# Kernel optimization log

Hardware: AMD Instinct MI355X
Metric: run time of the kernel (lower is better)

Reference implementation:

```python
import jax, jax.numpy as jnp
import numpy as np

N_HEAD = 12
NUM_CLUSTERS = 512
SCALE_FACTOR = 0.5
COEF_PRO = 0.3
EPS_COS = 1e-8


def _ln(x, g, b, eps=1e-5):
    m = jnp.mean(x, -1, keepdims=True)
    v = jnp.mean((x - m) ** 2, -1, keepdims=True)
    return (x - m) / jnp.sqrt(v + eps) * g + b


def _bn_gelu(y, g, b, eps=1e-5):
    # BatchNorm1d (training-mode batch stats) + exact GELU on (N, C)
    m = jnp.mean(y, 0)
    v = jnp.mean((y - m) ** 2, 0)
    return jax.nn.gelu((y - m) / jnp.sqrt(v + eps) * g + b, approximate=False)


def _quick_gelu(x):
    return x * jax.nn.sigmoid(1.702 * x)


def _seg_maxmean(f, idx, n):
    cnt = jax.ops.segment_sum(jnp.ones(f.shape[0], f.dtype), idx, n)
    s = jax.ops.segment_sum(f, idx, n)
    mx = jax.ops.segment_max(f, idx, n)
    mx = jnp.where(cnt[:, None] > 0, mx, 0.0)  # empty segments -> 0 (torch_scatter convention)
    mn = s / jnp.maximum(cnt, 1.0)[:, None]
    return mx, mn


def _cos(a, b):
    na = jnp.maximum(jnp.linalg.norm(a, axis=-1), EPS_COS)
    nb = jnp.maximum(jnp.linalg.norm(b, axis=-1), EPS_COS)
    return jnp.sum(a * b, -1) / (na * nb)


def _block(x, cluster, flat_grid_index, mask, grid_shape,
           ln1_g, ln1_b, w_qkv, b_qkv, w_o, b_o,
           ln2_g, ln2_b, w_fc, b_fc, w_proj, b_proj,
           w_down, b_down, w_up, b_up, bn3d_g, bn3d_b,
           n3_g, n3_b, vw_qkv, vb_qkv, vw_o, vb_o, bn1d_g, bn1d_b):
    B, S, C = x.shape
    G = S - 1
    Dh = C // N_HEAD
    # ---- multi-head self attention ----
    h = _ln(x, ln1_g, ln1_b)
    q, k, v = jnp.split(h @ w_qkv + b_qkv, 3, axis=-1)
    q = q.reshape(B, S, N_HEAD, Dh)
    k = k.reshape(B, S, N_HEAD, Dh)
    v = v.reshape(B, S, N_HEAD, Dh)
    scores = jnp.einsum('bqhd,bkhd->bhqk', q, k) / np.sqrt(Dh).astype(np.float32)
    attn = jax.nn.softmax(scores, -1)
    ao = jnp.einsum('bhqk,bkhd->bqhd', attn, v).reshape(B, S, C) @ w_o + b_o
    attn_weight = attn.mean(axis=1)  # averaged over heads, as need_weights=True
    x = x + ao
    # ---- MLP (QuickGELU) + adapter ----
    h2 = _ln(x, ln2_g, ln2_b)
    ffn = _quick_gelu(h2 @ w_fc + b_fc) @ w_proj + b_proj
    adp = jax.nn.gelu(ffn @ w_down + b_down, approximate=False) @ w_up + b_up
    x = x + ffn + SCALE_FACTOR * adp
    # ---- 3D cluster pooling ----
    cls_x = x[:, 0]
    xt = x[:, 1:]
    feat = xt.reshape(-1, C)
    mx, mn = _seg_maxmean(feat, cluster, NUM_CLUSTERS)
    x3d = _bn_gelu(mx + mn, bn3d_g, bn3d_b)[cluster].reshape(B, G, C)
    # ---- per-view 1D attention + grid scatter pooling ----
    V = mask.shape[0]
    D1 = B * grid_shape
    pos = []
    for i in range(V):
        y = _ln(feat, n3_g[i], n3_b[i]).reshape(B, G, C)
        q1, k1, v1 = jnp.split(y @ vw_qkv[i] + vb_qkv[i], 3, axis=-1)
        s1 = jnp.einsum('bqc,bkc->bqk', q1, k1) / np.sqrt(C).astype(np.float32)
        s1 = jnp.where(mask[i][:, None, :], s1, -1e9)
        a1 = jax.nn.softmax(s1, -1)
        o1 = jnp.einsum('bqk,bkc->bqc', a1, v1) @ vw_o[i] + vb_o[i]
        fx = o1.reshape(-1, C) + feat
        gi = flat_grid_index[i]
        mx1, mn1 = _seg_maxmean(fx, gi, D1)
        d2 = _bn_gelu(mn1 + mx1, bn1d_g[i], bn1d_b[i])[gi].reshape(B, G, C)
        pos.append(d2)
    x_sup = jnp.stack(pos, 0)                                   # (V,B,G,C)
    sims = jnp.stack([(_cos(p, x3d) + 1.0) / 2.0 for p in pos], 0)  # (V,B,G)
    sims = sims / sims.sum(0, keepdims=True)
    x_sup_w = jnp.einsum('vbg,vbgc->bgc', sims, x_sup)
    xt = xt + COEF_PRO * x_sup_w
    out = jnp.concatenate([cls_x[:, None], xt], 1)
    return out, attn_weight


def setup_inputs():
    B, S, C, V = 8, 1025, 768, 6
    GRID = 196
    G = S - 1
    key = jax.random.key(0)
    ks = iter(jax.random.split(key, 64))
    def w(shape):
        return jax.random.normal(next(ks), shape, jnp.float32) * 0.02
    return dict(
        x=jax.random.normal(next(ks), (B, S, C), jnp.float32),
        center1=jax.random.normal(next(ks), (B, V, 3), jnp.float32),
        cluster=jax.random.randint(next(ks), (B * G,), 0, NUM_CLUSTERS),
        flat_grid_index=jax.random.randint(next(ks), (V, B * G), 0, B * GRID),
        mask=jnp.ones((V, B, G), bool),
        grid_shape=GRID,
        ln1_g=jnp.ones(C), ln1_b=jnp.zeros(C),
        w_qkv=w((C, 3 * C)), b_qkv=jnp.zeros(3 * C),
        w_o=w((C, C)), b_o=jnp.zeros(C),
        ln2_g=jnp.ones(C), ln2_b=jnp.zeros(C),
        w_fc=w((C, 4 * C)), b_fc=jnp.zeros(4 * C),
        w_proj=w((4 * C, C)), b_proj=jnp.zeros(C),
        w_down=w((C, 16)), b_down=jnp.zeros(16),
        w_up=w((16, C)), b_up=jnp.zeros(C),
        bn3d_g=jnp.ones(C), bn3d_b=jnp.zeros(C),
        n3_g=jnp.ones((V, C)), n3_b=jnp.zeros((V, C)),
        vw_qkv=w((V, C, 3 * C)), vb_qkv=jnp.zeros((V, 3 * C)),
        vw_o=w((V, C, C)), vb_o=jnp.zeros((V, C)),
        bn1d_g=jnp.ones((V, C)), bn1d_b=jnp.zeros((V, C)),
    )


def reference(x, center1, cluster, flat_grid_index, mask, grid_shape,
              ln1_g, ln1_b, w_qkv, b_qkv, w_o, b_o,
              ln2_g, ln2_b, w_fc, b_fc, w_proj, b_proj,
              w_down, b_down, w_up, b_up, bn3d_g, bn3d_b,
              n3_g, n3_b, vw_qkv, vb_qkv, vw_o, vb_o, bn1d_g, bn1d_b):
    del center1  # only its shape (num_view) is used; V taken from mask
    return _block(x, cluster, flat_grid_index, mask, int(grid_shape),
                  ln1_g, ln1_b, w_qkv, b_qkv, w_o, b_o,
                  ln2_g, ln2_b, w_fc, b_fc, w_proj, b_proj,
                  w_down, b_down, w_up, b_up, bn3d_g, bn3d_b,
                  n3_g, n3_b, vw_qkv, vb_qkv, vw_o, vb_o, bn1d_g, bn1d_b)
```

## Files before the change

kernel.cpp:

```cpp
#include <hip/hip_runtime.h>
#include <math.h>
#include <float.h>

#define BATCH   8
#define SEQ     1025
#define GTOK    1024
#define CDIM    768
#define NHEAD   12
#define DHEAD   64
#define NVIEW   6
#define NCLUST  512
#define NGRID   1568
#define NROWS   8200
#define NFEAT   8192
#define SEGCAP  2048
#define LDT     1032
#define HG      3

typedef unsigned short bf16;
typedef __attribute__((ext_vector_type(8))) short bf16x8;
typedef __attribute__((ext_vector_type(4))) float f32x4;

__device__ __forceinline__ float b2f(bf16 u) {
    union { unsigned int i; float f; } v; v.i = ((unsigned int)u) << 16; return v.f;
}
__device__ __forceinline__ bf16 f2b(float f) {
    union { float f; unsigned int i; } v; v.f = f;
    unsigned int x = v.i;
    return (bf16)((x + 0x7fffu + ((x >> 16) & 1u)) >> 16);
}

__device__ __forceinline__ float block_reduce_sum(float v, float* red) {
    int tid = threadIdx.x;
    red[tid] = v; __syncthreads();
    for (int s = blockDim.x >> 1; s > 0; s >>= 1) {
        if (tid < s) red[tid] += red[tid + s];
        __syncthreads();
    }
    float r = red[0]; __syncthreads();
    return r;
}

__device__ __forceinline__ float brs_fast(float v, float* red4, int nw) {
    #pragma unroll
    for (int o = 32; o > 0; o >>= 1) v += __shfl_down(v, o);
    int lane = threadIdx.x & 63, wid = threadIdx.x >> 6;
    if (lane == 0) red4[wid] = v;
    __syncthreads();
    float r = 0.f;
    for (int i = 0; i < nw; ++i) r += red4[i];
    __syncthreads();
    return r;
}
__device__ __forceinline__ float brm_fast(float v, float* red4, int nw) {
    #pragma unroll
    for (int o = 32; o > 0; o >>= 1) v = fmaxf(v, __shfl_down(v, o));
    int lane = threadIdx.x & 63, wid = threadIdx.x >> 6;
    if (lane == 0) red4[wid] = v;
    __syncthreads();
    float r = -FLT_MAX;
    for (int i = 0; i < nw; ++i) r = fmaxf(r, red4[i]);
    __syncthreads();
    return r;
}

__device__ __forceinline__ float gelu_exact(float v) {
    return 0.5f * v * (1.f + erff(v * 0.70710678118654752f));
}
__device__ __forceinline__ float quick_gelu(float v) {
    return v / (1.f + expf(-1.702f * v));
}

__device__ __forceinline__ long long rmap(long long j, int remap) {
    return remap ? (j + 1 + (j >> 10)) : j;
}

__global__ __launch_bounds__(256)
void transpose_kernel(const float* __restrict__ W, bf16* __restrict__ WT, int K, int N)
{
    __shared__ float t[32][33];
    int n0 = blockIdx.x * 32, k0 = blockIdx.y * 32;
    int tx = threadIdx.x & 31, ty = threadIdx.x >> 5;
    #pragma unroll
    for (int i = 0; i < 4; ++i) {
        int k = k0 + ty + i * 8, n = n0 + tx;
        t[ty + i * 8][tx] = (k < K && n < N) ? W[(long long)k * N + n] : 0.f;
    }
    __syncthreads();
    #pragma unroll
    for (int i = 0; i < 4; ++i) {
        int n = n0 + ty + i * 8, k = k0 + tx;
        if (n < N && k < K)
            WT[(long long)n * K + k] = f2b(t[tx][ty + i * 8]);
    }
}

__global__ __launch_bounds__(256)
void transpose_bf16_kernel(const bf16* __restrict__ src, bf16* __restrict__ dst,
                           int K, int N, int lds, int ldd,
                           long long sSrc, long long sDst)
{
    __shared__ bf16 t[32][34];
    int z = blockIdx.z;
    const bf16* S = src + (long long)z * sSrc;
    bf16* D = dst + (long long)z * sDst;
    int n0 = blockIdx.x * 32, k0 = blockIdx.y * 32;
    int tx = threadIdx.x & 31, ty = threadIdx.x >> 5;
    #pragma unroll
    for (int i = 0; i < 4; ++i) {
        int k = k0 + ty + i * 8, n = n0 + tx;
        t[ty + i * 8][tx] = (k < K && n < N) ? S[(long long)k * lds + n] : (bf16)0;
    }
    __syncthreads();
    #pragma unroll
    for (int i = 0; i < 4; ++i) {
        int n = n0 + ty + i * 8, k = k0 + tx;
        if (n < N && k < K)
            D[(long long)n * ldd + k] = t[tx][ty + i * 8];
    }
}

__global__ __launch_bounds__(256)
void ln_kernel(const float* __restrict__ x, const float* __restrict__ g,
               const float* __restrict__ b, long long goff, bf16* __restrict__ out,
               int remap)
{
    __shared__ float red4[4];
    long long row = blockIdx.x;
    int tid = threadIdx.x;
    long long ibase = rmap(row, remap) * CDIM;
    long long obase = row * CDIM;
    float v0 = x[ibase + tid], v1 = x[ibase + tid + 256], v2 = x[ibase + tid + 512];
    float mean = brs_fast(v0 + v1 + v2, red4, 4) * (1.f / CDIM);
    float d0 = v0 - mean, d1 = v1 - mean, d2 = v2 - mean;
    float var = brs_fast(d0 * d0 + d1 * d1 + d2 * d2, red4, 4) * (1.f / CDIM);
    float rstd = rsqrtf(var + 1e-5f);
    bf16* orow = out + obase;
    orow[tid]       = f2b(d0 * rstd * g[goff + tid]       + b[goff + tid]);
    orow[tid + 256] = f2b(d1 * rstd * g[goff + tid + 256] + b[goff + tid + 256]);
    orow[tid + 512] = f2b(d2 * rstd * g[goff + tid + 512] + b[goff + tid + 512]);
}

#define LDSK 40

template<int TRANSB, int ATY, int OTY, int RES>
__global__ __launch_bounds__(256)
void gemm_k(const void* __restrict__ Av, const bf16* __restrict__ B,
            const float* __restrict__ bias, const float* __restrict__ Res,
            void* __restrict__ Cv,
            int M, int N, int K, int lda, int ldb, int ldc, int ldres,
            float alpha, int act, long long boff, long long biasoff, int zdiv,
            long long sA1, long long sA2, long long sB1, long long sB2,
            long long sC1, long long sC2, long long sRes)
{
    __shared__ short As[64][LDSK];
    __shared__ short Bs[64][LDSK];
    int bz = blockIdx.z;
    int bz1 = bz % zdiv, bz2 = bz / zdiv;
    int tid = threadIdx.x;
    int m0 = blockIdx.y * 64, n0 = blockIdx.x * 64;
    long long Aoff = bz1 * sA1 + bz2 * sA2;
    long long Boff = boff + bz1 * sB1 + bz2 * sB2;
    long long Coff = bz1 * sC1 + bz2 * sC2;
    long long Roff = bz1 * sRes;

    int lane = tid & 63;
    int w = tid >> 6;
    int wr = w >> 1, wc = w & 1;
    int fr = lane & 15;
    int kg = lane >> 4;

    f32x4 acc[2][2] = {};

    for (int k0 = 0; k0 < K; k0 += 32) {
        {
            int r = tid >> 2, kb = (tid & 3) * 8;
            int gm = m0 + r;
            short tmp[8] = {};
            if (gm < M) {
                long long base = Aoff + (long long)gm * lda + k0 + kb;
                if (k0 + kb + 8 <= K) {
                    if (ATY == 0) {
                        *reinterpret_cast<uint4*>(tmp) =
                            *reinterpret_cast<const uint4*>((const bf16*)Av + base);
                    } else {
                        float4 f0 = *reinterpret_cast<const float4*>((const float*)Av + base);
                        float4 f1 = *reinterpret_cast<const float4*>((const float*)Av + base + 4);
                        tmp[0]=(short)f2b(f0.x); tmp[1]=(short)f2b(f0.y);
                        tmp[2]=(short)f2b(f0.z); tmp[3]=(short)f2b(f0.w);
                        tmp[4]=(short)f2b(f1.x); tmp[5]=(short)f2b(f1.y);
                        tmp[6]=(short)f2b(f1.z); tmp[7]=(short)f2b(f1.w);
                    }
                } else {
                    #pragma unroll
                    for (int j = 0; j < 8; ++j) {
                        if (k0 + kb + j < K)
                            tmp[j] = ATY ? (short)f2b(((const float*)Av)[base + j])
                                         : (short)((const bf16*)Av)[base + j];
                    }
                }
            }
            *reinterpret_cast<uint4*>(&As[r][kb]) = *reinterpret_cast<uint4*>(tmp);
        }
        {
            int col = tid >> 2, kb = (tid & 3) * 8;
            int gn = n0 + col;
            short tmp[8] = {};
            if (gn < N) {
                if (TRANSB) {
                    long long base = Boff + (long long)gn * ldb + k0 + kb;
                    if (k0 + kb + 8 <= K) {
                        *reinterpret_cast<uint4*>(tmp) =
                            *reinterpret_cast<const uint4*>(B + base);
                    } else {
                        #pragma unroll
                        for (int j = 0; j < 8; ++j)
                            if (k0 + kb + j < K) tmp[j] = (short)B[base + j];
                    }
                } else {
                    #pragma unroll
                    for (int j = 0; j < 8; ++j) {
                        int kk = k0 + kb + j;
                        if (kk < K)
                            tmp[j] = (short)B[Boff + (long long)kk * ldb + gn];
                    }
                }
            }
            *reinterpret_cast<uint4*>(&Bs[col][kb]) = *reinterpret_cast<uint4*>(tmp);
        }
        __syncthreads();

        bf16x8 a0 = *reinterpret_cast<const bf16x8*>(&As[wr * 32 + fr][kg * 8]);
        bf16x8 a1 = *reinterpret_cast<const bf16x8*>(&As[wr * 32 + 16 + fr][kg * 8]);
        bf16x8 b0 = *reinterpret_cast<const bf16x8*>(&Bs[wc * 32 + fr][kg * 8]);
        bf16x8 b1 = *reinterpret_cast<const bf16x8*>(&Bs[wc * 32 + 16 + fr][kg * 8]);
        acc[0][0] = __builtin_amdgcn_mfma_f32_16x16x32_bf16(a0, b0, acc[0][0], 0, 0, 0);
        acc[0][1] = __builtin_amdgcn_mfma_f32_16x16x32_bf16(a0, b1, acc[0][1], 0, 0, 0);
        acc[1][0] = __builtin_amdgcn_mfma_f32_16x16x32_bf16(a1, b0, acc[1][0], 0, 0, 0);
        acc[1][1] = __builtin_amdgcn_mfma_f32_16x16x32_bf16(a1, b1, acc[1][1], 0, 0, 0);
        __syncthreads();
    }

    #pragma unroll
    for (int m = 0; m < 2; ++m) {
        #pragma unroll
        for (int n = 0; n < 2; ++n) {
            #pragma unroll
            for (int i = 0; i < 4; ++i) {
                int gm = m0 + wr * 32 + m * 16 + kg * 4 + i;
                int gn = n0 + wc * 32 + n * 16 + fr;
                if (gm >= M || gn >= N) continue;
                float v = acc[m][n][i] * alpha;
                if (bias) v += bias[biasoff + gn];
                if (act == 1) v = quick_gelu(v);
                if (RES) v += Res[Roff + (long long)gm * ldres + gn];
                long long ci = Coff + (long long)gm * ldc + gn;
                if (OTY) ((float*)Cv)[ci] = v;
                else     ((bf16*)Cv)[ci] = f2b(v);
            }
        }
    }
}

template<int TRANSB, int ATY, int OTY, int RES>
__global__ __launch_bounds__(512)
void gemm2(const void* __restrict__ Av, const bf16* __restrict__ B,
           const float* __restrict__ bias, const float* __restrict__ Res,
           void* __restrict__ Cv,
           int M, int N, int K, int lda, int ldb, int ldc, int ldres,
           float alpha, int act, long long boff, long long biasoff, int zdiv,
           long long sA1, long long sA2, long long sB1, long long sB2,
           long long sC1, long long sC2, long long sRes)
{
    __shared__ short As[128][LDSK];
    __shared__ short Bs[128][LDSK];
    int bz = blockIdx.z;
    int bz1 = bz % zdiv, bz2 = bz / zdiv;
    int tid = threadIdx.x;
    int m0 = blockIdx.y * 128, n0 = blockIdx.x * 128;
    long long Aoff = bz1 * sA1 + bz2 * sA2;
    long long Boff = boff + bz1 * sB1 + bz2 * sB2;
    long long Coff = bz1 * sC1 + bz2 * sC2;
    long long Roff = bz1 * sRes;

    int lane = tid & 63;
    int w = tid >> 6;
    int wr = w >> 2, wc = w & 3;
    int fr = lane & 15;
    int kg = lane >> 4;

    int srow = tid >> 2;
    int skb  = (tid & 3) * 8;

    short ra[8], rb[8];

    auto loadA = [&](int kk) {
        int gm = m0 + srow;
        if (gm < M) {
            long long base = Aoff + (long long)gm * lda + kk + skb;
            if (ATY == 0) {
                *reinterpret_cast<uint4*>(ra) =
                    *reinterpret_cast<const uint4*>((const bf16*)Av + base);
            } else {
                float4 f0 = *reinterpret_cast<const float4*>((const float*)Av + base);
                float4 f1 = *reinterpret_cast<const float4*>((const float*)Av + base + 4);
                ra[0]=(short)f2b(f0.x); ra[1]=(short)f2b(f0.y);
                ra[2]=(short)f2b(f0.z); ra[3]=(short)f2b(f0.w);
                ra[4]=(short)f2b(f1.x); ra[5]=(short)f2b(f1.y);
                ra[6]=(short)f2b(f1.z); ra[7]=(short)f2b(f1.w);
            }
        } else {
            #pragma unroll
            for (int j = 0; j < 8; ++j) ra[j] = 0;
        }
    };
    auto loadB = [&](int kk) {
        if (TRANSB) {
            int gn = n0 + srow;
            if (gn < N) {
                long long base = Boff + (long long)gn * ldb + kk + skb;
                *reinterpret_cast<uint4*>(rb) =
                    *reinterpret_cast<const uint4*>(B + base);
            } else {
                #pragma unroll
                for (int j = 0; j < 8; ++j) rb[j] = 0;
            }
        } else {
            int gn = n0 + srow;
            if (gn < N) {
                #pragma unroll
                for (int j = 0; j < 8; ++j) {
                    long long bi = Boff + (long long)(kk + skb + j) * ldb + gn;
                    rb[j] = (short)B[bi];
                }
            } else {
                #pragma unroll
                for (int j = 0; j < 8; ++j) rb[j] = 0;
            }
        }
    };

    f32x4 acc[4][2] = {};

    loadA(0); loadB(0);
    for (int k0 = 0; k0 < K; k0 += 32) {
        *reinterpret_cast<uint4*>(&As[srow][skb]) = *reinterpret_cast<uint4*>(ra);
        *reinterpret_cast<uint4*>(&Bs[srow][skb]) = *reinterpret_cast<uint4*>(rb);
        __syncthreads();
        if (k0 + 32 < K) { loadA(k0 + 32); loadB(k0 + 32); }

        bf16x8 a[4], bq[2];
        #pragma unroll
        for (int m = 0; m < 4; ++m)
            a[m] = *reinterpret_cast<const bf16x8*>(&As[wr * 64 + m * 16 + fr][kg * 8]);
        #pragma unroll
        for (int n = 0; n < 2; ++n)
            bq[n] = *reinterpret_cast<const bf16x8*>(&Bs[wc * 32 + n * 16 + fr][kg * 8]);
        #pragma unroll
        for (int m = 0; m < 4; ++m)
            #pragma unroll
            for (int n = 0; n < 2; ++n)
                acc[m][n] = __builtin_amdgcn_mfma_f32_16x16x32_bf16(a[m], bq[n], acc[m][n], 0, 0, 0);
        __syncthreads();
    }

    #pragma unroll
    for (int m = 0; m < 4; ++m) {
        #pragma unroll
        for (int n = 0; n < 2; ++n) {
            #pragma unroll
            for (int i = 0; i < 4; ++i) {
                int gm = m0 + wr * 64 + m * 16 + kg * 4 + i;
                int gn = n0 + wc * 32 + n * 16 + fr;
                if (gm >= M || gn >= N) continue;
                float v = acc[m][n][i] * alpha;
                if (bias) v += bias[biasoff + gn];
                if (act == 1) v = quick_gelu(v);
                if (RES) v += Res[Roff + (long long)gm * ldres + gn];
                long long ci = Coff + (long long)gm * ldc + gn;
                if (OTY) ((float*)Cv)[ci] = v;
                else     ((bf16*)Cv)[ci] = f2b(v);
            }
        }
    }
}

__global__ __launch_bounds__(256)
void softmax_aw3_kernel(bf16* __restrict__ T1, float* __restrict__ out, int first)
{
    __shared__ float red4[4];
    __shared__ float srow[SEQ];
    __shared__ float awsh[SEQ];
    long long r = blockIdx.x;
    float* aw = out + (long long)NROWS * CDIM + r * SEQ;
    int tid = threadIdx.x;
    const long long HSTRIDE = (long long)BATCH * SEQ * LDT;
    const float hscale = 1.f / (float)NHEAD;

    for (int k = tid; k < SEQ; k += 256) awsh[k] = 0.f;
    __syncthreads();

    for (int j = 0; j < HG; ++j) {
        bf16* sr = T1 + j * HSTRIDE + r * LDT;
        float lmax = -FLT_MAX;
        for (int k = tid; k < SEQ; k += 256) {
            float v = b2f(sr[k]);
            srow[k] = v;
            lmax = fmaxf(lmax, v);
        }
        __syncthreads();
        float m = brm_fast(lmax, red4, 4);

        float ls = 0.f;
        for (int k = tid; k < SEQ; k += 256) {
            float p = expf(srow[k] - m);
            srow[k] = p; ls += p;
        }
        float Z = brs_fast(ls, red4, 4);
        float inv = 1.f / fmaxf(Z, 1e-30f);
        for (int k = tid; k < SEQ; k += 256) {
            float p = srow[k] * inv;
            sr[k] = f2b(p);
            awsh[k] += p * hscale;
        }
        __syncthreads();
    }
    for (int k = tid; k < SEQ; k += 256)
        aw[k] = (first ? 0.f : aw[k]) + awsh[k];
}

__global__ __launch_bounds__(256)
void softmax_rows_bf16(bf16* __restrict__ s)
{
    __shared__ float red4[4];
    __shared__ float srow[GTOK];
    long long row = blockIdx.x;
    bf16* sr = s + row * GTOK;
    int tid = threadIdx.x;
    float lmax = -FLT_MAX;
    #pragma unroll
    for (int i = 0; i < 4; ++i) {
        float v = b2f(sr[tid + i * 256]);
        srow[tid + i * 256] = v;
        lmax = fmaxf(lmax, v);
    }
    __syncthreads();
    float m = brm_fast(lmax, red4, 4);
    float ls = 0.f;
    #pragma unroll
    for (int i = 0; i < 4; ++i) {
        float p = expf(srow[tid + i * 256] - m);
        srow[tid + i * 256] = p; ls += p;
    }
    float Z = brs_fast(ls, red4, 4);
    float inv = 1.f / fmaxf(Z, 1e-30f);
    #pragma unroll
    for (int i = 0; i < 4; ++i) sr[tid + i * 256] = f2b(srow[tid + i * 256] * inv);
}

__global__ __launch_bounds__(256)
void adp_final_kernel(const bf16* __restrict__ ffn, const float* __restrict__ w_down,
                      const float* __restrict__ b_down, const float* __restrict__ w_up,
                      const float* __restrict__ b_up, const float* __restrict__ x2,
                      float* __restrict__ out)
{
    __shared__ float rowsh[CDIM];
    __shared__ float red[256];
    __shared__ float a[16];
    long long row = blockIdx.x;
    int tid = threadIdx.x;
    for (int c = tid; c < CDIM; c += 256) rowsh[c] = b2f(ffn[row * CDIM + c]);
    __syncthreads();
    int n = tid & 15;
    int part = tid >> 4;
    float s = 0.f;
    for (int i = part; i < CDIM; i += 16) s += rowsh[i] * w_down[i * 16 + n];
    red[tid] = s; __syncthreads();
    if (tid < 16) {
        float t = 0.f;
        #pragma unroll
        for (int p = 0; p < 16; ++p) t += red[p * 16 + tid];
        a[tid] = gelu_exact(t + b_down[tid]);
    }
    __syncthreads();

    #pragma unroll
    for (int i = 0; i < 3; ++i) {
        int c = tid + i * 256;
        float acc = b_up[c];
        #pragma unroll
        for (int k = 0; k < 16; ++k) acc += a[k] * w_up[k * CDIM + c];
        out[row * CDIM + c] = x2[row * CDIM + c] + rowsh[c] + 0.5f * acc;
    }
}

__global__ __launch_bounds__(256)
void seg_kernel(const float* __restrict__ feat, const int* __restrict__ idx,
                float* __restrict__ y, int remap)
{
    __shared__ int sidx[NFEAT];
    __shared__ int list[SEGCAP];
    __shared__ int offs[256];
    int seg = blockIdx.x;
    int tid = threadIdx.x;
    for (int j = tid; j < NFEAT; j += 256) sidx[j] = idx[j];
    __syncthreads();

    int base = tid * 32;
    int cnt = 0;
    #pragma unroll
    for (int i = 0; i < 32; ++i) cnt += (sidx[base + i] == seg) ? 1 : 0;
    offs[tid] = cnt;
    __syncthreads();
    for (int st = 1; st < 256; st <<= 1) {
        int v = (tid >= st) ? offs[tid - st] : 0;
        __syncthreads();
        offs[tid] += v;
        __syncthreads();
    }
    int total = offs[255];
    int pos = offs[tid] - cnt;
    __syncthreads();

    float mx0 = -FLT_MAX, mx1 = -FLT_MAX, mx2 = -FLT_MAX;
    float s0 = 0.f, s1 = 0.f, s2 = 0.f;

    if (total <= SEGCAP) {
        #pragma unroll
        for (int i = 0; i < 32; ++i) {
            int j = base + i;
            if (sidx[j] == seg) list[pos++] = j;
        }
        __syncthreads();
        for (int i = 0; i < total; ++i) {
            const float* fr = feat + rmap(list[i], remap) * CDIM;
            float v0 = fr[tid], v1 = fr[tid + 256], v2 = fr[tid + 512];
            s0 += v0; s1 += v1; s2 += v2;
            mx0 = fmaxf(mx0, v0); mx1 = fmaxf(mx1, v1); mx2 = fmaxf(mx2, v2);
        }
    } else {
        for (int j = 0; j < NFEAT; ++j) {
            if (sidx[j] == seg) {
                const float* fr = feat + rmap(j, remap) * CDIM;
                float v0 = fr[tid], v1 = fr[tid + 256], v2 = fr[tid + 512];
                s0 += v0; s1 += v1; s2 += v2;
                mx0 = fmaxf(mx0, v0); mx1 = fmaxf(mx1, v1); mx2 = fmaxf(mx2, v2);
            }
        }
    }

    if (total == 0) { mx0 = mx1 = mx2 = 0.f; }
    float inv = 1.f / (float)(total > 0 ? total : 1);
    float* yr = y + (long long)seg * CDIM;
    yr[tid]       = mx0 + s0 * inv;
    yr[tid + 256] = mx1 + s1 * inv;
    yr[tid + 512] = mx2 + s2 * inv;
}

__global__ __launch_bounds__(128)
void bn_gelu_kernel(const float* __restrict__ y, const float* __restrict__ g,
                    const float* __restrict__ b, long long goff,
                    bf16* __restrict__ out, int R)
{
    __shared__ float red4[4];
    int c = blockIdx.x;
    int tid = threadIdx.x;
    float s = 0.f;
    for (int r = tid; r < R; r += 128) s += y[(long long)r * CDIM + c];
    float mean = brs_fast(s, red4, 2) / (float)R;
    float ss = 0.f;
    for (int r = tid; r < R; r += 128) {
        float d = y[(long long)r * CDIM + c] - mean;
        ss += d * d;
    }
    float var = fmaxf(brs_fast(ss, red4, 2) / (float)R, 0.f);
    float rstd = rsqrtf(var + 1e-5f);
    float gc = g[goff + c], bc = b[goff + c];
    for (int r = tid; r < R; r += 128) {
        float v = (y[(long long)r * CDIM + c] - mean) * rstd * gc + bc;
        out[(long long)r * CDIM + c] = f2b(gelu_exact(v));
    }
}

__global__ __launch_bounds__(256)
void fuse_final_kernel(const bf16* __restrict__ bn3d, const bf16* __restrict__ bn1d,
                       const int* __restrict__ cluster, const int* __restrict__ fgi,
                       float* __restrict__ out)
{
    __shared__ float red4[4];
    __shared__ float x3s[CDIM];
    __shared__ bf16 pc[NVIEW][CDIM];
    __shared__ float simsh[NVIEW];
    int j = blockIdx.x;
    int tid = threadIdx.x;
    int b = j >> 10, g = j & 1023;
    const bf16* x3 = bn3d + (long long)cluster[j] * CDIM;
    float s = 0.f;
    for (int c = tid; c < CDIM; c += 256) {
        float v = b2f(x3[c]);
        x3s[c] = v;
        s += v * v;
    }
    __syncthreads();
    float nx3 = fmaxf(sqrtf(brs_fast(s, red4, 4)), 1e-8f);

    for (int i = 0; i < NVIEW; ++i) {
        const bf16* p = bn1d + ((long long)i * NGRID + fgi[i * NFEAT + j]) * CDIM;
        float d = 0.f, nn = 0.f;
        for (int c = tid; c < CDIM; c += 256) {
            bf16 u = p[c];
            pc[i][c] = u;
            float pv = b2f(u);
            d += pv * x3s[c]; nn += pv * pv;
        }
        float D = brs_fast(d, red4, 4);
        float Np = sqrtf(brs_fast(nn, red4, 4));
        if (tid == 0) {
            float cosv = D / (fmaxf(Np, 1e-8f) * nx3);
            simsh[i] = (cosv + 1.f) * 0.5f;
        }
    }
    __syncthreads();
    float ssum = 0.f;
    #pragma unroll
    for (int i = 0; i < NVIEW; ++i) ssum += simsh[i];
    float invs = 1.f / fmaxf(ssum, 1e-20f);
    long long orow = ((long long)b * SEQ + 1 + g) * CDIM;
    for (int c = tid; c < CDIM; c += 256) {
        float acc = 0.f;
        #pragma unroll
        for (int i = 0; i < NVIEW; ++i) acc += simsh[i] * invs * b2f(pc[i][c]);
        out[orow + c] = out[orow + c] + 0.3f * acc;
    }
}

extern "C" void kernel_launch(void* const* d_in, const int* in_sizes, int n_in,
                              void* d_out, int out_size, void* d_ws, size_t ws_size,
                              hipStream_t stream)
{
    const float* x      = (const float*)d_in[0];
    const int*  cluster = (const int*)d_in[2];
    const int*  fgi     = (const int*)d_in[3];
    const float* ln1_g = (const float*)d_in[6];
    const float* ln1_b = (const float*)d_in[7];
    const float* w_qkv = (const float*)d_in[8];
    const float* b_qkv = (const float*)d_in[9];
    const float* w_o   = (const float*)d_in[10];
    const float* b_o   = (const float*)d_in[11];
    const float* ln2_g = (const float*)d_in[12];
    const float* ln2_b = (const float*)d_in[13];
    const float* w_fc  = (const float*)d_in[14];
    const float* b_fc  = (const float*)d_in[15];
    const float* w_proj= (const float*)d_in[16];
    const float* b_proj= (const float*)d_in[17];
    const float* w_down= (const float*)d_in[18];
    const float* b_down= (const float*)d_in[19];
    const float* w_up  = (const float*)d_in[20];
    const float* b_up  = (const float*)d_in[21];
    const float* bn3d_g= (const float*)d_in[22];
    const float* bn3d_b= (const float*)d_in[23];
    const float* n3_g  = (const float*)d_in[24];
    const float* n3_b  = (const float*)d_in[25];
    const float* vw_qkv= (const float*)d_in[26];
    const float* vb_qkv= (const float*)d_in[27];
    const float* vw_o  = (const float*)d_in[28];
    const float* vb_o  = (const float*)d_in[29];
    const float* bn1d_g= (const float*)d_in[30];
    const float* bn1d_b= (const float*)d_in[31];
    (void)in_sizes; (void)n_in; (void)out_size; (void)ws_size;

    float* out = (float*)d_out;

    char* w = (char*)d_ws;
    bf16*  QKV    = (bf16*)w;  w += (long long)NROWS * 3 * CDIM * 2;
    bf16*  H      = (bf16*)w;  w += (long long)NROWS * CDIM * 2;
    float* X2     = (float*)w; w += (long long)NROWS * CDIM * 4;
    bf16*  AO     = (bf16*)w;  w += (long long)NROWS * CDIM * 2;
    bf16*  FFN    = (bf16*)w;  w += (long long)NROWS * CDIM * 2;
    float* T1     = (float*)w; w += (long long)HG * BATCH * SEQ * LDT * 2;
    float* Y512   = (float*)w; w += (long long)NCLUST * CDIM * 4;
    bf16*  BN3D   = (bf16*)w;  w += (long long)NCLUST * CDIM * 2;
    float* YG     = (float*)w; w += (long long)NGRID * CDIM * 4;
    bf16*  BN1D   = (bf16*)w;  w += (long long)NVIEW * NGRID * CDIM * 2;
    bf16*  WQKVT  = (bf16*)w;  w += (long long)(3*CDIM) * CDIM * 2;
    bf16*  WOT    = (bf16*)w;  w += (long long)CDIM * CDIM * 2;
    bf16*  WFCT   = (bf16*)w;  w += (long long)(4*CDIM) * CDIM * 2;
    bf16*  WPROJT = (bf16*)w;  w += (long long)CDIM * (4*CDIM) * 2;
    bf16*  VWQKVT = (bf16*)w;  w += (long long)(3*CDIM) * CDIM * 2;
    bf16*  VWOT   = (bf16*)w;  w += (long long)CDIM * CDIM * 2;
    bf16*  VT     = (bf16*)w;  w += (long long)BATCH * CDIM * LDT * 2;
    bf16*  T1b    = (bf16*)T1;

    dim3 blk(256), blk512(512);

    transpose_kernel<<<dim3(72, 24), blk, 0, stream>>>(w_qkv, WQKVT, CDIM, 3*CDIM);
    transpose_kernel<<<dim3(24, 24), blk, 0, stream>>>(w_o, WOT, CDIM, CDIM);
    transpose_kernel<<<dim3(96, 24), blk, 0, stream>>>(w_fc, WFCT, CDIM, 4*CDIM);
    transpose_kernel<<<dim3(24, 96), blk, 0, stream>>>(w_proj, WPROJT, 4*CDIM, CDIM);

    ln_kernel<<<NROWS, blk, 0, stream>>>(x, ln1_g, ln1_b, 0LL, H, 0);

    gemm2<1,0,0,0><<<dim3(18, 65, 1), blk512, 0, stream>>>(
        H, WQKVT, b_qkv, nullptr, QKV,
        NROWS, 3*CDIM, CDIM, CDIM, CDIM, 3*CDIM, 0, 1.f, 0, 0LL, 0LL,
        1, 0, 0, 0, 0, 0, 0, 0);

    transpose_bf16_kernel<<<dim3(24, 33, BATCH), blk, 0, stream>>>(
        QKV + 2*CDIM, VT, SEQ, CDIM, 3*CDIM, LDT,
        (long long)SEQ * 3*CDIM, (long long)CDIM * LDT);

    const long long HSTR = (long long)BATCH * SEQ * LDT;
    for (int g = 0; g < NHEAD / HG; ++g) {
        int hb = g * HG;
        gemm2<1,0,0,0><<<dim3(9, 9, BATCH * HG), blk512, 0, stream>>>(
            QKV + hb * DHEAD, QKV + CDIM + hb * DHEAD, nullptr, nullptr, T1b,
            SEQ, SEQ, DHEAD, 3*CDIM, 3*CDIM, LDT, 0, 0.125f, 0, 0LL, 0LL,
            BATCH, (long long)SEQ * 3*CDIM, DHEAD,
            (long long)SEQ * 3*CDIM, DHEAD,
            (long long)SEQ * LDT, HSTR, 0);

        softmax_aw3_kernel<<<NROWS, blk, 0, stream>>>(T1b, out, g == 0 ? 1 : 0);

        gemm_k<1,0,0,0><<<dim3(1, 17, BATCH * HG), blk, 0, stream>>>(
            T1b, VT + (long long)hb * DHEAD * LDT, nullptr, nullptr, AO + hb * DHEAD,
            SEQ, DHEAD, SEQ, LDT, LDT, CDIM, 0, 1.f, 0, 0LL, 0LL,
            BATCH, (long long)SEQ * LDT, HSTR,
            (long long)CDIM * LDT, (long long)DHEAD * LDT,
            (long long)SEQ * CDIM, DHEAD, 0);
    }

    gemm2<1,0,1,1><<<dim3(6, 65, 1), blk512, 0, stream>>>(
        AO, WOT, b_o, x, X2,
        NROWS, CDIM, CDIM, CDIM, CDIM, CDIM, CDIM, 1.f, 0, 0LL, 0LL,
        1, 0, 0, 0, 0, 0, 0, 0);

    ln_kernel<<<NROWS, blk, 0, stream>>>(X2, ln2_g, ln2_b, 0LL, H, 0);

    {
        bf16* MID = (bf16*)T1;
        for (int cidx = 0; cidx < 2; ++cidx) {
            long long r0 = 4100LL * cidx;
            int m = 4100;
            gemm2<1,0,0,0><<<dim3(24, 33, 1), blk512, 0, stream>>>(
                H + r0 * CDIM, WFCT, b_fc, nullptr, MID,
                m, 4*CDIM, CDIM, CDIM, CDIM, 4*CDIM, 0, 1.f, 1, 0LL, 0LL,
                1, 0, 0, 0, 0, 0, 0, 0);
            gemm2<1,0,0,0><<<dim3(6, 33, 1), blk512, 0, stream>>>(
                MID, WPROJT, b_proj, nullptr, FFN + r0 * CDIM,
                m, CDIM, 4*CDIM, 4*CDIM, 4*CDIM, CDIM, 0, 1.f, 0, 0LL, 0LL,
                1, 0, 0, 0, 0, 0, 0, 0);
        }
    }

    adp_final_kernel<<<NROWS, blk, 0, stream>>>(FFN, w_down, b_down, w_up, b_up,
                                                X2, out);

    seg_kernel<<<NCLUST, blk, 0, stream>>>(out, cluster, Y512, 1);
    bn_gelu_kernel<<<CDIM, dim3(128), 0, stream>>>(Y512, bn3d_g, bn3d_b, 0LL, BN3D, NCLUST);

    const float inv_sqrt_c = 0.03608439182435161f;
    for (int i = 0; i < NVIEW; ++i) {
        transpose_kernel<<<dim3(72, 24), blk, 0, stream>>>(
            vw_qkv + (long long)i * CDIM * 3*CDIM, VWQKVT, CDIM, 3*CDIM);
        transpose_kernel<<<dim3(24, 24), blk, 0, stream>>>(
            vw_o + (long long)i * CDIM * CDIM, VWOT, CDIM, CDIM);

        ln_kernel<<<NFEAT, blk, 0, stream>>>(out, n3_g, n3_b, (long long)i * CDIM, H, 1);

        gemm2<1,0,0,0><<<dim3(18, 64, 1), blk512, 0, stream>>>(
            H, VWQKVT, vb_qkv, nullptr, QKV,
            NFEAT, 3*CDIM, CDIM, CDIM, CDIM, 3*CDIM, 0, 1.f, 0,
            0LL, (long long)i * 3*CDIM, 1, 0, 0, 0, 0, 0, 0, 0);

        transpose_bf16_kernel<<<dim3(24, 32, BATCH), blk, 0, stream>>>(
            QKV + 2*CDIM, VT, GTOK, CDIM, 3*CDIM, GTOK,
            (long long)GTOK * 3*CDIM, (long long)CDIM * GTOK);

        gemm2<1,0,0,0><<<dim3(8, 8, BATCH), blk512, 0, stream>>>(
            QKV, QKV + CDIM, nullptr, nullptr, T1b,
            GTOK, GTOK, CDIM, 3*CDIM, 3*CDIM, GTOK, 0, inv_sqrt_c, 0, 0LL, 0LL,
            BATCH, (long long)GTOK * 3*CDIM, 0,
            (long long)GTOK * 3*CDIM, 0,
            (long long)GTOK * GTOK, 0, 0);

        softmax_rows_bf16<<<BATCH * GTOK, blk, 0, stream>>>(T1b);

        gemm2<1,0,0,0><<<dim3(6, 8, BATCH), blk512, 0, stream>>>(
            T1b, VT, nullptr, nullptr, AO,
            GTOK, CDIM, GTOK, GTOK, GTOK, CDIM, 0, 1.f, 0, 0LL, 0LL,
            BATCH, (long long)GTOK * GTOK, 0,
            (long long)CDIM * GTOK, 0,
            (long long)GTOK * CDIM, 0, 0);

        gemm2<1,0,1,1><<<dim3(6, 8, BATCH), blk512, 0, stream>>>(
            AO, VWOT, vb_o, out + CDIM, X2,
            GTOK, CDIM, CDIM, CDIM, CDIM, CDIM, CDIM, 1.f, 0,
            0LL, (long long)i * CDIM,
            BATCH, (long long)GTOK * CDIM, 0, 0, 0,
            (long long)GTOK * CDIM, 0, (long long)SEQ * CDIM);

        seg_kernel<<<NGRID, blk, 0, stream>>>(X2, fgi + i * NFEAT, YG, 0);
        bn_gelu_kernel<<<CDIM, dim3(128), 0, stream>>>(
            YG, bn1d_g, bn1d_b, (long long)i * CDIM,
            BN1D + (long long)i * NGRID * CDIM, NGRID);
    }

    fuse_final_kernel<<<NFEAT, blk, 0, stream>>>(BN3D, BN1D, cluster, fgi, out);
}
```

Baseline: 2.556 ms.

## Hoist view LayerNorm out of loop, split BatchNorm into coalesced passes, unsplit MLP

The per-view LayerNorm is replaced by a single normalisation pass before the view loop. The per-view gamma/beta affine is folded into the A-operand load of the QKV GEMM, so the 6 per-view LN launches become one. The column-strided bn_gelu kernel is replaced by partial-sum, stat and apply kernels with coalesced row-major access. Variance now comes from E[x^2]-mean^2, which is less numerically stable. The MLP GEMMs also run in one launch instead of two row chunks, and the per-element affine in the GEMM load adds scalar work and an extra bf16 rounding.

Measured after the change: 2.439 ms. 4.6% less time.

```diff
diff --git a/kernel.cpp b/kernel.cpp
--- a/kernel.cpp
+++ b/kernel.cpp
@@ -16,6 +16,7 @@
 #define SEGCAP  2048
 #define LDT     1032
 #define HG      3
+#define BNCH    16
 
 typedef unsigned short bf16;
 typedef __attribute__((ext_vector_type(8))) short bf16x8;
@@ -139,6 +140,25 @@
     orow[tid]       = f2b(d0 * rstd * g[goff + tid]       + b[goff + tid]);
     orow[tid + 256] = f2b(d1 * rstd * g[goff + tid + 256] + b[goff + tid + 256]);
     orow[tid + 512] = f2b(d2 * rstd * g[goff + tid + 512] + b[goff + tid + 512]);
+}
+
+__global__ __launch_bounds__(256)
+void norm_kernel(const float* __restrict__ x, bf16* __restrict__ out)
+{
+    __shared__ float red4[4];
+    long long row = blockIdx.x;
+    int tid = threadIdx.x;
+    long long ibase = rmap(row, 1) * CDIM;
+    long long obase = row * CDIM;
+    float v0 = x[ibase + tid], v1 = x[ibase + tid + 256], v2 = x[ibase + tid + 512];
+    float mean = brs_fast(v0 + v1 + v2, red4, 4) * (1.f / CDIM);
+    float d0 = v0 - mean, d1 = v1 - mean, d2 = v2 - mean;
+    float var = brs_fast(d0 * d0 + d1 * d1 + d2 * d2, red4, 4) * (1.f / CDIM);
+    float rstd = rsqrtf(var + 1e-5f);
+    bf16* orow = out + obase;
+    orow[tid]       = f2b(d0 * rstd);
+    orow[tid + 256] = f2b(d1 * rstd);
+    orow[tid + 512] = f2b(d2 * rstd);
 }
 
 #define LDSK 40
@@ -262,7 +282,7 @@
     }
 }
 
-template<int TRANSB, int ATY, int OTY, int RES>
+template<int TRANSB, int ATY, int OTY, int RES, int ASC>
 __global__ __launch_bounds__(512)
 void gemm2(const void* __restrict__ Av, const bf16* __restrict__ B,
            const float* __restrict__ bias, const float* __restrict__ Res,
@@ -270,7 +290,9 @@
            int M, int N, int K, int lda, int ldb, int ldc, int ldres,
            float alpha, int act, long long boff, long long biasoff, int zdiv,
            long long sA1, long long sA2, long long sB1, long long sB2,
-           long long sC1, long long sC2, long long sRes)
+           long long sC1, long long sC2, long long sRes,
+           const float* __restrict__ gsc, const float* __restrict__ gbs,
+           long long gsoff)
 {
     __shared__ short As[128][LDSK];
     __shared__ short Bs[128][LDSK];
@@ -301,6 +323,13 @@
             if (ATY == 0) {
                 *reinterpret_cast<uint4*>(ra) =
                     *reinterpret_cast<const uint4*>((const bf16*)Av + base);
+                if (ASC) {
+                    #pragma unroll
+                    for (int j = 0; j < 8; ++j) {
+                        long long gi = gsoff + kk + skb + j;
+                        ra[j] = (short)f2b(b2f((bf16)ra[j]) * gsc[gi] + gbs[gi]);
+                    }
+                }
             } else {
                 float4 f0 = *reinterpret_cast<const float4*>((const float*)Av + base);
                 float4 f1 = *reinterpret_cast<const float4*>((const float*)Av + base + 4);
@@ -557,28 +586,58 @@
     yr[tid + 512] = mx2 + s2 * inv;
 }
 
-__global__ __launch_bounds__(128)
-void bn_gelu_kernel(const float* __restrict__ y, const float* __restrict__ g,
-                    const float* __restrict__ b, long long goff,
-                    bf16* __restrict__ out, int R)
-{
-    __shared__ float red4[4];
-    int c = blockIdx.x;
-    int tid = threadIdx.x;
-    float s = 0.f;
-    for (int r = tid; r < R; r += 128) s += y[(long long)r * CDIM + c];
-    float mean = brs_fast(s, red4, 2) / (float)R;
-    float ss = 0.f;
-    for (int r = tid; r < R; r += 128) {
-        float d = y[(long long)r * CDIM + c] - mean;
-        ss += d * d;
-    }
-    float var = fmaxf(brs_fast(ss, red4, 2) / (float)R, 0.f);
-    float rstd = rsqrtf(var + 1e-5f);
-    float gc = g[goff + c], bc = b[goff + c];
-    for (int r = tid; r < R; r += 128) {
-        float v = (y[(long long)r * CDIM + c] - mean) * rstd * gc + bc;
-        out[(long long)r * CDIM + c] = f2b(gelu_exact(v));
+__global__ __launch_bounds__(256)
+void bn_part_kernel(const float* __restrict__ y, float* __restrict__ part, int R)
+{
+    __shared__ float sh[2][4][64];
+    int cb = blockIdx.x * 64;
+    int ch = blockIdx.y;
+    int r0 = (R * ch) / BNCH, r1 = (R * (ch + 1)) / BNCH;
+    int tx = threadIdx.x & 63, ty = threadIdx.x >> 6;
+    int c = cb + tx;
+    float s = 0.f, ss = 0.f;
+    for (int r = r0 + ty; r < r1; r += 4) {
+        float v = y[(long long)r * CDIM + c];
+        s += v; ss += v * v;
+    }
+    sh[0][ty][tx] = s; sh[1][ty][tx] = ss;
+    __syncthreads();
+    if (ty == 0) {
+        float S  = sh[0][0][tx] + sh[0][1][tx] + sh[0][2][tx] + sh[0][3][tx];
+        float SS = sh[1][0][tx] + sh[1][1][tx] + sh[1][2][tx] + sh[1][3][tx];
+        part[(long long)ch * CDIM * 2 + c]        = S;
+        part[(long long)ch * CDIM * 2 + CDIM + c] = SS;
+    }
+}
+
+__global__ __launch_bounds__(256)
+void bn_stat_kernel(const float* __restrict__ part, float* __restrict__ meanr, int R)
+{
+    int c = blockIdx.x * 256 + threadIdx.x;
+    if (c >= CDIM) return;
+    float S = 0.f, SS = 0.f;
+    for (int ch = 0; ch < BNCH; ++ch) {
+        S  += part[(long long)ch * CDIM * 2 + c];
+        SS += part[(long long)ch * CDIM * 2 + CDIM + c];
+    }
+    float mean = S / (float)R;
+    float var = fmaxf(SS / (float)R - mean * mean, 0.f);
+    meanr[c] = mean;
+    meanr[CDIM + c] = rsqrtf(var + 1e-5f);
+}
+
+__global__ __launch_bounds__(256)
+void bn_apply_kernel(const float* __restrict__ y, const float* __restrict__ meanr,
+                     const float* __restrict__ g, const float* __restrict__ b,
+                     long long goff, bf16* __restrict__ out)
+{
+    long long r = blockIdx.x;
+    int tid = threadIdx.x;
+    #pragma unroll
+    for (int i = 0; i < 3; ++i) {
+        int c = tid + i * 256;
+        float v = (y[r * CDIM + c] - meanr[c]) * meanr[CDIM + c] * g[goff + c] + b[goff + c];
+        out[r * CDIM + c] = f2b(gelu_exact(v));
     }
 }
 
@@ -689,6 +748,8 @@
     bf16*  VWQKVT = (bf16*)w;  w += (long long)(3*CDIM) * CDIM * 2;
     bf16*  VWOT   = (bf16*)w;  w += (long long)CDIM * CDIM * 2;
     bf16*  VT     = (bf16*)w;  w += (long long)BATCH * CDIM * LDT * 2;
+    float* BPART  = (float*)w; w += (long long)BNCH * CDIM * 2 * 4;
+    float* BSTAT  = (float*)w; w += (long long)CDIM * 2 * 4;
     bf16*  T1b    = (bf16*)T1;
 
     dim3 blk(256), blk512(512);
@@ -700,10 +761,10 @@
 
     ln_kernel<<<NROWS, blk, 0, stream>>>(x, ln1_g, ln1_b, 0LL, H, 0);
 
-    gemm2<1,0,0,0><<<dim3(18, 65, 1), blk512, 0, stream>>>(
+    gemm2<1,0,0,0,0><<<dim3(18, 65, 1), blk512, 0, stream>>>(
         H, WQKVT, b_qkv, nullptr, QKV,
         NROWS, 3*CDIM, CDIM, CDIM, CDIM, 3*CDIM, 0, 1.f, 0, 0LL, 0LL,
-        1, 0, 0, 0, 0, 0, 0, 0);
+        1, 0, 0, 0, 0, 0, 0, 0, nullptr, nullptr, 0);
 
     transpose_bf16_kernel<<<dim3(24, 33, BATCH), blk, 0, stream>>>(
         QKV + 2*CDIM, VT, SEQ, CDIM, 3*CDIM, LDT,
@@ -712,12 +773,12 @@
     const long long HSTR = (long long)BATCH * SEQ * LDT;
     for (int g = 0; g < NHEAD / HG; ++g) {
         int hb = g * HG;
-        gemm2<1,0,0,0><<<dim3(9, 9, BATCH * HG), blk512, 0, stream>>>(
+        gemm2<1,0,0,0,0><<<dim3(9, 9, BATCH * HG), blk512, 0, stream>>>(
             QKV + hb * DHEAD, QKV + CDIM + hb * DHEAD, nullptr, nullptr, T1b,
             SEQ, SEQ, DHEAD, 3*CDIM, 3*CDIM, LDT, 0, 0.125f, 0, 0LL, 0LL,
             BATCH, (long long)SEQ * 3*CDIM, DHEAD,
             (long long)SEQ * 3*CDIM, DHEAD,
-            (long long)SEQ * LDT, HSTR, 0);
+            (long long)SEQ * LDT, HSTR, 0, nullptr, nullptr, 0);
 
         softmax_aw3_kernel<<<NROWS, blk, 0, stream>>>(T1b, out, g == 0 ? 1 : 0);
 
@@ -729,34 +790,34 @@
             (long long)SEQ * CDIM, DHEAD, 0);
     }
 
-    gemm2<1,0,1,1><<<dim3(6, 65, 1), blk512, 0, stream>>>(
+    gemm2<1,0,1,1,0><<<dim3(6, 65, 1), blk512, 0, stream>>>(
         AO, WOT, b_o, x, X2,
         NROWS, CDIM, CDIM, CDIM, CDIM, CDIM, CDIM, 1.f, 0, 0LL, 0LL,
-        1, 0, 0, 0, 0, 0, 0, 0);
+        1, 0, 0, 0, 0, 0, 0, 0, nullptr, nullptr, 0);
 
     ln_kernel<<<NROWS, blk, 0, stream>>>(X2, ln2_g, ln2_b, 0LL, H, 0);
 
     {
         bf16* MID = (bf16*)T1;
-        for (int cidx = 0; cidx < 2; ++cidx) {
-            long long r0 = 4100LL * cidx;
-            int m = 4100;
-            gemm2<1,0,0,0><<<dim3(24, 33, 1), blk512, 0, stream>>>(
-                H + r0 * CDIM, WFCT, b_fc, nullptr, MID,
-                m, 4*CDIM, CDIM, CDIM, CDIM, 4*CDIM, 0, 1.f, 1, 0LL, 0LL,
-                1, 0, 0, 0, 0, 0, 0, 0);
-            gemm2<1,0,0,0><<<dim3(6, 33, 1), blk512, 0, stream>>>(
-                MID, WPROJT, b_proj, nullptr, FFN + r0 * CDIM,
-                m, CDIM, 4*CDIM, 4*CDIM, 4*CDIM, CDIM, 0, 1.f, 0, 0LL, 0LL,
-                1, 0, 0, 0, 0, 0, 0, 0);
-        }
+        gemm2<1,0,0,0,0><<<dim3(24, 65, 1), blk512, 0, stream>>>(
+            H, WFCT, b_fc, nullptr, MID,
+            NROWS, 4*CDIM, CDIM, CDIM, CDIM, 4*CDIM, 0, 1.f, 1, 0LL, 0LL,
+            1, 0, 0, 0, 0, 0, 0, 0, nullptr, nullptr, 0);
+        gemm2<1,0,0,0,0><<<dim3(6, 65, 1), blk512, 0, stream>>>(
+            MID, WPROJT, b_proj, nullptr, FFN,
+            NROWS, CDIM, 4*CDIM, 4*CDIM, 4*CDIM, CDIM, 0, 1.f, 0, 0LL, 0LL,
+            1, 0, 0, 0, 0, 0, 0, 0, nullptr, nullptr, 0);
     }
 
     adp_final_kernel<<<NROWS, blk, 0, stream>>>(FFN, w_down, b_down, w_up, b_up,
                                                 X2, out);
 
+    norm_kernel<<<NFEAT, blk, 0, stream>>>(out, H);
+
     seg_kernel<<<NCLUST, blk, 0, stream>>>(out, cluster, Y512, 1);
-    bn_gelu_kernel<<<CDIM, dim3(128), 0, stream>>>(Y512, bn3d_g, bn3d_b, 0LL, BN3D, NCLUST);
+    bn_part_kernel<<<dim3(12, BNCH), blk, 0, stream>>>(Y512, BPART, NCLUST);
+    bn_stat_kernel<<<dim3(3), blk, 0, stream>>>(BPART, BSTAT, NCLUST);
+    bn_apply_kernel<<<NCLUST, blk, 0, stream>>>(Y512, BSTAT, bn3d_g, bn3d_b, 0LL, BN3D);
 
     const float inv_sqrt_c = 0.03608439182435161f;
     for (int i = 0; i < NVIEW; ++i) {
@@ -765,44 +826,45 @@
         transpose_kernel<<<dim3(24, 24), blk, 0, stream>>>(
             vw_o + (long long)i * CDIM * CDIM, VWOT, CDIM, CDIM);
 
-        ln_kernel<<<NFEAT, blk, 0, stream>>>(out, n3_g, n3_b, (long long)i * CDIM, H, 1);
-
-        gemm2<1,0,0,0><<<dim3(18, 64, 1), blk512, 0, stream>>>(
+        gemm2<1,0,0,0,1><<<dim3(18, 64, 1), blk512, 0, stream>>>(
             H, VWQKVT, vb_qkv, nullptr, QKV,
             NFEAT, 3*CDIM, CDIM, CDIM, CDIM, 3*CDIM, 0, 1.f, 0,
-            0LL, (long long)i * 3*CDIM, 1, 0, 0, 0, 0, 0, 0, 0);
+            0LL, (long long)i * 3*CDIM, 1, 0, 0, 0, 0, 0, 0, 0,
+            n3_g, n3_b, (long long)i * CDIM);
 
         transpose_bf16_kernel<<<dim3(24, 32, BATCH), blk, 0, stream>>>(
             QKV + 2*CDIM, VT, GTOK, CDIM, 3*CDIM, GTOK,
             (long long)GTOK * 3*CDIM, (long long)CDIM * GTOK);
 
-        gemm2<1,0,0,0><<<dim3(8, 8, BATCH), blk512, 0, stream>>>(
+        gemm2<1,0,0,0,0><<<dim3(8, 8, BATCH), blk512, 0, stream>>>(
             QKV, QKV + CDIM, nullptr, nullptr, T1b,
             GTOK, GTOK, CDIM, 3*CDIM, 3*CDIM, GTOK, 0, inv_sqrt_c, 0, 0LL, 0LL,
             BATCH, (long long)GTOK * 3*CDIM, 0,
             (long long)GTOK * 3*CDIM, 0,
-            (long long)GTOK * GTOK, 0, 0);
+            (long long)GTOK * GTOK, 0, 0, nullptr, nullptr, 0);
 
         softmax_rows_bf16<<<BATCH * GTOK, blk, 0, stream>>>(T1b);
 
-        gemm2<1,0,0,0><<<dim3(6, 8, BATCH), blk512, 0, stream>>>(
+        gemm2<1,0,0,0,0><<<dim3(6, 8, BATCH), blk512, 0, stream>>>(
             T1b, VT, nullptr, nullptr, AO,
             GTOK, CDIM, GTOK, GTOK, GTOK, CDIM, 0, 1.f, 0, 0LL, 0LL,
             BATCH, (long long)GTOK * GTOK, 0,
             (long long)CDIM * GTOK, 0,
-            (long long)GTOK * CDIM, 0, 0);
-
-        gemm2<1,0,1,1><<<dim3(6, 8, BATCH), blk512, 0, stream>>>(
+            (long long)GTOK * CDIM, 0, 0, nullptr, nullptr, 0);
+
+        gemm2<1,0,1,1,0><<<dim3(6, 8, BATCH), blk512, 0, stream>>>(
             AO, VWOT, vb_o, out + CDIM, X2,
             GTOK, CDIM, CDIM, CDIM, CDIM, CDIM, CDIM, 1.f, 0,
             0LL, (long long)i * CDIM,
             BATCH, (long long)GTOK * CDIM, 0, 0, 0,
-            (long long)GTOK * CDIM, 0, (long long)SEQ * CDIM);
+            (long long)GTOK * CDIM, 0, (long long)SEQ * CDIM, nullptr, nullptr, 0);
 
         seg_kernel<<<NGRID, blk, 0, stream>>>(X2, fgi + i * NFEAT, YG, 0);
-        bn_gelu_kernel<<<CDIM, dim3(128), 0, stream>>>(
-            YG, bn1d_g, bn1d_b, (long long)i * CDIM,
-            BN1D + (long long)i * NGRID * CDIM, NGRID);
+        bn_part_kernel<<<dim3(12, BNCH), blk, 0, stream>>>(YG, BPART, NGRID);
+        bn_stat_kernel<<<dim3(3), blk, 0, stream>>>(BPART, BSTAT, NGRID);
+        bn_apply_kernel<<<NGRID, blk, 0, stream>>>(YG, BSTAT, bn1d_g, bn1d_b,
+                                                   (long long)i * CDIM,
+                                                   BN1D + (long long)i * NGRID * CDIM);
     }
 
     fuse_final_kernel<<<NFEAT, blk, 0, stream>>>(BN3D, BN1D, cluster, fgi, out);
```
